# Kernel optimization log

Hardware: AMD Instinct MI355X
Metric: run time of the kernel (lower is better)

## Reference

```python
import jax, jax.numpy as jnp
import numpy as np

C = 192

def _dw_conv(x, w, k):
    # x: [B, C, H, W]; w: [C, 1, k, k]; depthwise => feature_group_count=C
    pad = k // 2
    return jax.lax.conv_general_dilated(
        x, w,
        window_strides=(1, 1),
        padding=[(pad, pad), (pad, pad)],
        dimension_numbers=("NCHW", "OIHW", "NCHW"),
        feature_group_count=x.shape[1],
    )

def setup_inputs() -> dict:
    key = jax.random.key(0)
    k1, k2, k3 = jax.random.split(key, 3)
    x = jax.random.normal(k1, (32, C, 64, 64), dtype=jnp.float32)
    # depthwise kernels: (out_ch=C, in_ch/groups=1, kh, kw), fan_in-style scaling
    w5 = jax.random.normal(k2, (C, 1, 5, 5), dtype=jnp.float32) * (1.0 / 5.0)
    w51 = jax.random.normal(k3, (C, 1, 51, 51), dtype=jnp.float32) * (1.0 / 51.0)
    return {"x": x, "w5": w5, "w51": w51}

def reference(x, w5, w51):
    # out = dw5(x) + dw51(x)
    return _dw_conv(x, w5, 5) + _dw_conv(x, w51, 51)
```

## Files before the change

### kernel.cpp

```cpp
#include <hip/hip_runtime.h>

typedef __bf16 bf16x8 __attribute__((ext_vector_type(8)));
typedef float  f32x16 __attribute__((ext_vector_type(16)));

__device__ __forceinline__ unsigned short f2bf_bits(float f) {
    unsigned int u = __builtin_bit_cast(unsigned int, f);
    u += 0x7FFFu + ((u >> 16) & 1u);
    return (unsigned short)(u >> 16);
}

__global__ void __launch_bounds__(256, 2) dw5_51_kernel(
    const float* __restrict__ x,
    const float* __restrict__ w5,
    const float* __restrict__ w51,
    float* __restrict__ out)
{
    __shared__ unsigned short wlds[8 * 1024];
    __shared__ unsigned short rowbuf[4][2][1088];

    const int tid = threadIdx.x;
    const int wg  = blockIdx.x;
    const int c   = wg >> 2;
    const int bg  = wg & 3;

    {
        const int s    = tid >> 1;
        const int half = tid & 1;
        const int kh   = 88 - s;
        const bool rowok = (kh >= 0) && (kh <= 50);
        #pragma unroll
        for (int j = 0; j < 32; ++j) {
            const int kw = half * 32 + j;
            float v = 0.0f;
            if (rowok && kw <= 50) {
                v = w51[c * 2601 + kh * 51 + kw];
                if (kh >= 23 && kh < 28 && kw >= 23 && kw < 28)
                    v += w5[c * 25 + (kh - 23) * 5 + (kw - 23)];
            }
            wlds[(kw >> 3) * 1024 + s * 8 + (kw & 7)] = f2bf_bits(v);
        }
    }

    const int lane = tid & 63;
    const int wv   = tid >> 6;
    const int b0   = bg * 8 + wv * 2;
    const int n32  = lane & 31;
    const int gg   = lane >> 5;
    const int q    = lane & 7;
    const int u8   = n32 >> 3;

    {
        unsigned int* z = (unsigned int*)&rowbuf[wv][0][0];
        #pragma unroll
        for (int i = 0; i < 17; ++i) z[lane + 64 * i] = 0u;
    }
    __syncthreads();

    const long ib0 = ((long)b0 * 192 + c) * 4096;
    const long ib1 = ib0 + 192L * 4096;
    const float* xr0 = x + ib0 + lane;
    const float* xr1 = x + ib1 + lane;

    const int bidx  = 136 * q + 8 * u8 + 8 * gg;
    const int wbase = lane + 25;
    const int abase = gg * 1024 + n32 * 8;

    unsigned short* rb0 = &rowbuf[wv][0][0];
    unsigned short* rb1 = &rowbuf[wv][1][0];

    f32x16 acc[2][2][2] = {};
    bf16x8 A[2][4];
    bf16x8 d0[6], d1[6];

    auto R1 = [&](int r) {
        const int s0 = (63 - r) * 8 + abase;
        const int s1 = (95 - r) * 8 + abase;
        #pragma unroll
        for (int ks = 0; ks < 2; ++ks) {
            A[0][ks] = *(const bf16x8*)&wlds[s0 + ks * 2048];
            A[1][ks] = *(const bf16x8*)&wlds[s1 + ks * 2048];
        }
        #pragma unroll
        for (int t = 0; t < 4; ++t) {
            d0[t] = *(const bf16x8*)&rb0[bidx + 16 * t];
            d1[t] = *(const bf16x8*)&rb1[bidx + 16 * t];
        }
    };
    auto R2 = [&](int r) {
        const int s0 = (63 - r) * 8 + abase;
        const int s1 = (95 - r) * 8 + abase;
        #pragma unroll
        for (int ks = 2; ks < 4; ++ks) {
            A[0][ks] = *(const bf16x8*)&wlds[s0 + ks * 2048];
            A[1][ks] = *(const bf16x8*)&wlds[s1 + ks * 2048];
        }
        #pragma unroll
        for (int t = 4; t < 6; ++t) {
            d0[t] = *(const bf16x8*)&rb0[bidx + 16 * t];
            d1[t] = *(const bf16x8*)&rb1[bidx + 16 * t];
        }
    };
    auto MF1 = [&](int r) {
        __builtin_amdgcn_s_setprio(1);
        if (r <= 56) {
            #pragma unroll
            for (int ks = 0; ks < 2; ++ks) {
                acc[0][0][0] = __builtin_amdgcn_mfma_f32_32x32x16_bf16(A[0][ks], d0[ks],     acc[0][0][0], 0, 0, 0);
                acc[0][0][1] = __builtin_amdgcn_mfma_f32_32x32x16_bf16(A[0][ks], d0[ks + 2], acc[0][0][1], 0, 0, 0);
                acc[1][0][0] = __builtin_amdgcn_mfma_f32_32x32x16_bf16(A[0][ks], d1[ks],     acc[1][0][0], 0, 0, 0);
                acc[1][0][1] = __builtin_amdgcn_mfma_f32_32x32x16_bf16(A[0][ks], d1[ks + 2], acc[1][0][1], 0, 0, 0);
            }
        }
        if (r >= 7) {
            #pragma unroll
            for (int ks = 0; ks < 2; ++ks) {
                acc[0][1][0] = __builtin_amdgcn_mfma_f32_32x32x16_bf16(A[1][ks], d0[ks],     acc[0][1][0], 0, 0, 0);
                acc[0][1][1] = __builtin_amdgcn_mfma_f32_32x32x16_bf16(A[1][ks], d0[ks + 2], acc[0][1][1], 0, 0, 0);
                acc[1][1][0] = __builtin_amdgcn_mfma_f32_32x32x16_bf16(A[1][ks], d1[ks],     acc[1][1][0], 0, 0, 0);
                acc[1][1][1] = __builtin_amdgcn_mfma_f32_32x32x16_bf16(A[1][ks], d1[ks + 2], acc[1][1][1], 0, 0, 0);
            }
        }
    };
    auto MF2 = [&](int r) {
        if (r <= 56) {
            #pragma unroll
            for (int ks = 2; ks < 4; ++ks) {
                acc[0][0][0] = __builtin_amdgcn_mfma_f32_32x32x16_bf16(A[0][ks], d0[ks],     acc[0][0][0], 0, 0, 0);
                acc[0][0][1] = __builtin_amdgcn_mfma_f32_32x32x16_bf16(A[0][ks], d0[ks + 2], acc[0][0][1], 0, 0, 0);
                acc[1][0][0] = __builtin_amdgcn_mfma_f32_32x32x16_bf16(A[0][ks], d1[ks],     acc[1][0][0], 0, 0, 0);
                acc[1][0][1] = __builtin_amdgcn_mfma_f32_32x32x16_bf16(A[0][ks], d1[ks + 2], acc[1][0][1], 0, 0, 0);
            }
        }
        if (r >= 7) {
            #pragma unroll
            for (int ks = 2; ks < 4; ++ks) {
                acc[0][1][0] = __builtin_amdgcn_mfma_f32_32x32x16_bf16(A[1][ks], d0[ks],     acc[0][1][0], 0, 0, 0);
                acc[0][1][1] = __builtin_amdgcn_mfma_f32_32x32x16_bf16(A[1][ks], d0[ks + 2], acc[0][1][1], 0, 0, 0);
                acc[1][1][0] = __builtin_amdgcn_mfma_f32_32x32x16_bf16(A[1][ks], d1[ks],     acc[1][1][0], 0, 0, 0);
                acc[1][1][1] = __builtin_amdgcn_mfma_f32_32x32x16_bf16(A[1][ks], d1[ks + 2], acc[1][1][1], 0, 0, 0);
            }
        }
        __builtin_amdgcn_s_setprio(0);
    };
    auto W = [&](float v0, float v1) {
        const unsigned short w0 = f2bf_bits(v0), w1 = f2bf_bits(v1);
        #pragma unroll
        for (int qq = 0; qq < 8; ++qq) {
            rb0[wbase + 135 * qq] = w0;
            rb1[wbase + 135 * qq] = w1;
        }
    };

    float xv0 = xr0[0], xv1 = xr1[0];
    W(xv0, xv1);
    R1(0);
    R2(0);
    xv0 = xr0[64]; xv1 = xr1[64];

    #pragma unroll 1
    for (int i = 0; i < 63; ++i) {
        MF1(i);
        MF2(i);
        __builtin_amdgcn_sched_barrier(0);
        W(xv0, xv1);
        R1(i + 1);
        R2(i + 1);
        if (i + 2 < 64) { xv0 = xr0[(i + 2) * 64]; xv1 = xr1[(i + 2) * 64]; }
        __builtin_amdgcn_sched_barrier(0);
    }
    MF1(63);
    MF2(63);

    float* outp0 = out + ib0;
    float* outp1 = out + ib1;
    #pragma unroll
    for (int v = 0; v < 16; ++v) {
        const int ho = (v & 3) + 8 * (v >> 2) + 4 * gg;
        outp0[ho * 64 + n32]             = acc[0][0][0][v];
        outp0[ho * 64 + n32 + 32]        = acc[0][0][1][v];
        outp0[(ho + 32) * 64 + n32]      = acc[0][1][0][v];
        outp0[(ho + 32) * 64 + n32 + 32] = acc[0][1][1][v];
        outp1[ho * 64 + n32]             = acc[1][0][0][v];
        outp1[ho * 64 + n32 + 32]        = acc[1][0][1][v];
        outp1[(ho + 32) * 64 + n32]      = acc[1][1][0][v];
        outp1[(ho + 32) * 64 + n32 + 32] = acc[1][1][1][v];
    }
}

extern "C" void kernel_launch(void* const* d_in, const int* in_sizes, int n_in,
                              void* d_out, int out_size, void* d_ws, size_t ws_size,
                              hipStream_t stream) {
    (void)in_sizes; (void)n_in; (void)d_ws; (void)ws_size; (void)out_size;
    const float* x   = (const float*)d_in[0];
    const float* w5  = (const float*)d_in[1];
    const float* w51 = (const float*)d_in[2];
    float* out = (float*)d_out;
    dim3 grid(192 * 4), block(256);
    hipLaunchKernelGGL(dw5_51_kernel, grid, block, 0, stream, x, w5, w51, out);
}
```

Before: 163.0 us.

## Process one image per wave and double grid to raise occupancy

Each wave now handles a single batch image instead of two. This halves the accumulator and row-buffer registers and the LDS row buffer, and the grid doubles to 1536 blocks with launch bounds raised to 3 blocks per CU. The goal is more resident waves to hide LDS and global latency. In exchange, each block reloads and converts the full 51x51 weight tile twice as often, and each weight fragment read from LDS feeds half as many MFMAs, which raises LDS traffic per unit of work.

```diff
diff --git a/kernel.cpp b/kernel.cpp
--- a/kernel.cpp
+++ b/kernel.cpp
@@ -9,19 +9,19 @@
     return (unsigned short)(u >> 16);
 }
 
-__global__ void __launch_bounds__(256, 2) dw5_51_kernel(
+__global__ void __launch_bounds__(256, 3) dw5_51_kernel(
     const float* __restrict__ x,
     const float* __restrict__ w5,
     const float* __restrict__ w51,
     float* __restrict__ out)
 {
     __shared__ unsigned short wlds[8 * 1024];
-    __shared__ unsigned short rowbuf[4][2][1088];
+    __shared__ unsigned short rowbuf[4][1088];
 
     const int tid = threadIdx.x;
     const int wg  = blockIdx.x;
-    const int c   = wg >> 2;
-    const int bg  = wg & 3;
+    const int c   = wg >> 3;
+    const int bg  = wg & 7;
 
     {
         const int s    = tid >> 1;
@@ -43,34 +43,32 @@
 
     const int lane = tid & 63;
     const int wv   = tid >> 6;
-    const int b0   = bg * 8 + wv * 2;
+    const int b    = bg * 4 + wv;
     const int n32  = lane & 31;
     const int gg   = lane >> 5;
     const int q    = lane & 7;
     const int u8   = n32 >> 3;
 
     {
-        unsigned int* z = (unsigned int*)&rowbuf[wv][0][0];
+        unsigned int* z = (unsigned int*)&rowbuf[wv][0];
         #pragma unroll
-        for (int i = 0; i < 17; ++i) z[lane + 64 * i] = 0u;
+        for (int i = 0; i < 8; ++i) z[lane + 64 * i] = 0u;
+        if (lane < 32) z[lane + 512] = 0u;
     }
     __syncthreads();
 
-    const long ib0 = ((long)b0 * 192 + c) * 4096;
-    const long ib1 = ib0 + 192L * 4096;
-    const float* xr0 = x + ib0 + lane;
-    const float* xr1 = x + ib1 + lane;
+    const long imgbase = ((long)b * 192 + c) * 4096;
+    const float* xrow = x + imgbase + lane;
 
     const int bidx  = 136 * q + 8 * u8 + 8 * gg;
     const int wbase = lane + 25;
     const int abase = gg * 1024 + n32 * 8;
 
-    unsigned short* rb0 = &rowbuf[wv][0][0];
-    unsigned short* rb1 = &rowbuf[wv][1][0];
+    unsigned short* rb = &rowbuf[wv][0];
 
-    f32x16 acc[2][2][2] = {};
+    f32x16 acc00 = {}, acc01 = {}, acc10 = {}, acc11 = {};
     bf16x8 A[2][4];
-    bf16x8 d0[6], d1[6];
+    bf16x8 d[6];
 
     auto R1 = [&](int r) {
         const int s0 = (63 - r) * 8 + abase;
@@ -81,10 +79,7 @@
             A[1][ks] = *(const bf16x8*)&wlds[s1 + ks * 2048];
         }
         #pragma unroll
-        for (int t = 0; t < 4; ++t) {
-            d0[t] = *(const bf16x8*)&rb0[bidx + 16 * t];
-            d1[t] = *(const bf16x8*)&rb1[bidx + 16 * t];
-        }
+        for (int t = 0; t < 4; ++t) d[t] = *(const bf16x8*)&rb[bidx + 16 * t];
     };
     auto R2 = [&](int r) {
         const int s0 = (63 - r) * 8 + abase;
@@ -95,29 +90,22 @@
             A[1][ks] = *(const bf16x8*)&wlds[s1 + ks * 2048];
         }
         #pragma unroll
-        for (int t = 4; t < 6; ++t) {
-            d0[t] = *(const bf16x8*)&rb0[bidx + 16 * t];
-            d1[t] = *(const bf16x8*)&rb1[bidx + 16 * t];
-        }
+        for (int t = 4; t < 6; ++t) d[t] = *(const bf16x8*)&rb[bidx + 16 * t];
     };
     auto MF1 = [&](int r) {
         __builtin_amdgcn_s_setprio(1);
         if (r <= 56) {
             #pragma unroll
             for (int ks = 0; ks < 2; ++ks) {
-                acc[0][0][0] = __builtin_amdgcn_mfma_f32_32x32x16_bf16(A[0][ks], d0[ks],     acc[0][0][0], 0, 0, 0);
-                acc[0][0][1] = __builtin_amdgcn_mfma_f32_32x32x16_bf16(A[0][ks], d0[ks + 2], acc[0][0][1], 0, 0, 0);
-                acc[1][0][0] = __builtin_amdgcn_mfma_f32_32x32x16_bf16(A[0][ks], d1[ks],     acc[1][0][0], 0, 0, 0);
-                acc[1][0][1] = __builtin_amdgcn_mfma_f32_32x32x16_bf16(A[0][ks], d1[ks + 2], acc[1][0][1], 0, 0, 0);
+                acc00 = __builtin_amdgcn_mfma_f32_32x32x16_bf16(A[0][ks], d[ks],     acc00, 0, 0, 0);
+                acc01 = __builtin_amdgcn_mfma_f32_32x32x16_bf16(A[0][ks], d[ks + 2], acc01, 0, 0, 0);
             }
         }
         if (r >= 7) {
             #pragma unroll
             for (int ks = 0; ks < 2; ++ks) {
-                acc[0][1][0] = __builtin_amdgcn_mfma_f32_32x32x16_bf16(A[1][ks], d0[ks],     acc[0][1][0], 0, 0, 0);
-                acc[0][1][1] = __builtin_amdgcn_mfma_f32_32x32x16_bf16(A[1][ks], d0[ks + 2], acc[0][1][1], 0, 0, 0);
-                acc[1][1][0] = __builtin_amdgcn_mfma_f32_32x32x16_bf16(A[1][ks], d1[ks],     acc[1][1][0], 0, 0, 0);
-                acc[1][1][1] = __builtin_amdgcn_mfma_f32_32x32x16_bf16(A[1][ks], d1[ks + 2], acc[1][1][1], 0, 0, 0);
+                acc10 = __builtin_amdgcn_mfma_f32_32x32x16_bf16(A[1][ks], d[ks],     acc10, 0, 0, 0);
+                acc11 = __builtin_amdgcn_mfma_f32_32x32x16_bf16(A[1][ks], d[ks + 2], acc11, 0, 0, 0);
             }
         }
     };
@@ -125,65 +113,53 @@
         if (r <= 56) {
             #pragma unroll
             for (int ks = 2; ks < 4; ++ks) {
-                acc[0][0][0] = __builtin_amdgcn_mfma_f32_32x32x16_bf16(A[0][ks], d0[ks],     acc[0][0][0], 0, 0, 0);
-                acc[0][0][1] = __builtin_amdgcn_mfma_f32_32x32x16_bf16(A[0][ks], d0[ks + 2], acc[0][0][1], 0, 0, 0);
-                acc[1][0][0] = __builtin_amdgcn_mfma_f32_32x32x16_bf16(A[0][ks], d1[ks],     acc[1][0][0], 0, 0, 0);
-                acc[1][0][1] = __builtin_amdgcn_mfma_f32_32x32x16_bf16(A[0][ks], d1[ks + 2], acc[1][0][1], 0, 0, 0);
+                acc00 = __builtin_amdgcn_mfma_f32_32x32x16_bf16(A[0][ks], d[ks],     acc00, 0, 0, 0);
+                acc01 = __builtin_amdgcn_mfma_f32_32x32x16_bf16(A[0][ks], d[ks + 2], acc01, 0, 0, 0);
             }
         }
         if (r >= 7) {
             #pragma unroll
             for (int ks = 2; ks < 4; ++ks) {
-                acc[0][1][0] = __builtin_amdgcn_mfma_f32_32x32x16_bf16(A[1][ks], d0[ks],     acc[0][1][0], 0, 0, 0);
-                acc[0][1][1] = __builtin_amdgcn_mfma_f32_32x32x16_bf16(A[1][ks], d0[ks + 2], acc[0][1][1], 0, 0, 0);
-                acc[1][1][0] = __builtin_amdgcn_mfma_f32_32x32x16_bf16(A[1][ks], d1[ks],     acc[1][1][0], 0, 0, 0);
-                acc[1][1][1] = __builtin_amdgcn_mfma_f32_32x32x16_bf16(A[1][ks], d1[ks + 2], acc[1][1][1], 0, 0, 0);
+                acc10 = __builtin_amdgcn_mfma_f32_32x32x16_bf16(A[1][ks], d[ks],     acc10, 0, 0, 0);
+                acc11 = __builtin_amdgcn_mfma_f32_32x32x16_bf16(A[1][ks], d[ks + 2], acc11, 0, 0, 0);
             }
         }
         __builtin_amdgcn_s_setprio(0);
     };
-    auto W = [&](float v0, float v1) {
-        const unsigned short w0 = f2bf_bits(v0), w1 = f2bf_bits(v1);
+    auto W = [&](float v) {
+        const unsigned short w0 = f2bf_bits(v);
         #pragma unroll
-        for (int qq = 0; qq < 8; ++qq) {
-            rb0[wbase + 135 * qq] = w0;
-            rb1[wbase + 135 * qq] = w1;
-        }
+        for (int qq = 0; qq < 8; ++qq) rb[wbase + 135 * qq] = w0;
     };
 
-    float xv0 = xr0[0], xv1 = xr1[0];
-    W(xv0, xv1);
+    float xv = xrow[0];
+    W(xv);
     R1(0);
     R2(0);
-    xv0 = xr0[64]; xv1 = xr1[64];
+    xv = xrow[64];
 
     #pragma unroll 1
     for (int i = 0; i < 63; ++i) {
         MF1(i);
         MF2(i);
         __builtin_amdgcn_sched_barrier(0);
-        W(xv0, xv1);
+        W(xv);
         R1(i + 1);
         R2(i + 1);
-        if (i + 2 < 64) { xv0 = xr0[(i + 2) * 64]; xv1 = xr1[(i + 2) * 64]; }
+        if (i + 2 < 64) xv = xrow[(i + 2) * 64];
         __builtin_amdgcn_sched_barrier(0);
     }
     MF1(63);
     MF2(63);
 
-    float* outp0 = out + ib0;
-    float* outp1 = out + ib1;
+    float* outp = out + imgbase;
     #pragma unroll
     for (int v = 0; v < 16; ++v) {
         const int ho = (v & 3) + 8 * (v >> 2) + 4 * gg;
-        outp0[ho * 64 + n32]             = acc[0][0][0][v];
-        outp0[ho * 64 + n32 + 32]        = acc[0][0][1][v];
-        outp0[(ho + 32) * 64 + n32]      = acc[0][1][0][v];
-        outp0[(ho + 32) * 64 + n32 + 32] = acc[0][1][1][v];
-        outp1[ho * 64 + n32]             = acc[1][0][0][v];
-        outp1[ho * 64 + n32 + 32]        = acc[1][0][1][v];
-        outp1[(ho + 32) * 64 + n32]      = acc[1][1][0][v];
-        outp1[(ho + 32) * 64 + n32 + 32] = acc[1][1][1][v];
+        outp[ho * 64 + n32]             = acc00[v];
+        outp[ho * 64 + n32 + 32]        = acc01[v];
+        outp[(ho + 32) * 64 + n32]      = acc10[v];
+        outp[(ho + 32) * 64 + n32 + 32] = acc11[v];
     }
 }
 
@@ -195,6 +171,6 @@
     const float* w5  = (const float*)d_in[1];
     const float* w51 = (const float*)d_in[2];
     float* out = (float*)d_out;
-    dim3 grid(192 * 4), block(256);
+    dim3 grid(192 * 8), block(256);
     hipLaunchKernelGGL(dw5_51_kernel, grid, block, 0, stream, x, w5, w51, out);
 }
```

After: 143.8 us. 1.13x faster.
